# Kernel optimization log

Measured on AMD Instinct MI355X. Metric: run time of the kernel, lower is better.

## Reference

```python
import jax, jax.numpy as jnp
import numpy as np

D = 1024        # n_embed
POS = 512       # n_pos_embed
H = 16          # heads
HS = D // H     # head size
DFF = 4 * D     # mlp hidden
EPS = 1e-5


def layernorm(x, g, b, eps=EPS):
    mu = jnp.mean(x, axis=-1, keepdims=True)
    var = jnp.var(x, axis=-1, keepdims=True)
    return (x - mu) * jax.lax.rsqrt(var + eps) * g + b


def setup_inputs() -> dict:
    key = jax.random.key(0)
    ks = jax.random.split(key, 12)
    std = 0.02
    inp = {
        "grid": jax.random.normal(ks[0], (8, 24, 24, D), dtype=jnp.float32),
        "query_pos": jax.random.normal(ks[1], (8, 1024, POS), dtype=jnp.float32),
        "Wq": jax.random.normal(ks[2], (POS, D), dtype=jnp.float32) * std,
        "Wk": jax.random.normal(ks[3], (D, D), dtype=jnp.float32) * std,
        "Wv": jax.random.normal(ks[4], (D, D), dtype=jnp.float32) * std,
        "Wo": jax.random.normal(ks[5], (D, D), dtype=jnp.float32) * std,
        "ln_grid_g": jnp.ones((D,), jnp.float32),
        "ln_grid_b": jnp.zeros((D,), jnp.float32),
        "ln_q_g": jnp.ones((POS,), jnp.float32),
        "ln_q_b": jnp.zeros((POS,), jnp.float32),
        "ln_mlp_g": jnp.ones((D,), jnp.float32),
        "ln_mlp_b": jnp.zeros((D,), jnp.float32),
        "W1": jax.random.normal(ks[6], (D, DFF), dtype=jnp.float32) * std,
        "b1": jnp.zeros((DFF,), jnp.float32),
        "W2": jax.random.normal(ks[7], (DFF, D), dtype=jnp.float32) * std,
        "b2": jnp.zeros((D,), jnp.float32),
    }
    return inp


def reference(grid, query_pos, Wq, Wk, Wv, Wo, ln_grid_g, ln_grid_b,
              ln_q_g, ln_q_b, ln_mlp_g, ln_mlp_b, W1, b1, W2, b2):
    B, N, M, d = grid.shape
    T = N * M
    grid_flat = grid.reshape(B, T, d)
    grid_norm = layernorm(grid_flat, ln_grid_g, ln_grid_b)
    K = jnp.einsum('btd,de->bte', grid_norm, Wk)
    V = jnp.einsum('btd,de->bte', grid_norm, Wv)
    query_norm = layernorm(query_pos, ln_q_g, ln_q_b)
    Q = jnp.einsum('blp,pe->ble', query_norm, Wq)
    L = Q.shape[1]
    # split heads: (B, H, L, HS)
    Qh = Q.reshape(B, L, H, HS).transpose(0, 2, 1, 3)
    Kh = K.reshape(B, T, H, HS).transpose(0, 2, 1, 3)
    Vh = V.reshape(B, T, H, HS).transpose(0, 2, 1, 3)
    scale = 1.0 / np.sqrt(HS).astype(np.float32)
    scores = jnp.einsum('bhld,bhmd->bhlm', Qh, Kh) * scale
    probs = jax.nn.softmax(scores, axis=-1)
    attn = jnp.einsum('bhlm,bhmd->bhld', probs, Vh)
    attn = attn.transpose(0, 2, 1, 3).reshape(B, L, d)
    attn = jnp.einsum('bld,de->ble', attn, Wo)
    x = Q + attn  # Q_proj residual
    x_norm = layernorm(x, ln_mlp_g, ln_mlp_b)
    mlp = jax.nn.gelu(x_norm @ W1 + b1) @ W2 + b2
    return x + mlp
```

## Files before the change

kernel.cpp:

```cpp
#include <hip/hip_runtime.h>

typedef __bf16 bf16x8 __attribute__((ext_vector_type(8)));
typedef float  f32x4  __attribute__((ext_vector_type(4)));
typedef short  s16x8  __attribute__((ext_vector_type(8)));

__device__ __forceinline__ unsigned short f2b(float f) {
  unsigned int u = __float_as_uint(f);
  u += 0x7fffu + ((u >> 16) & 1u);
  return (unsigned short)(u >> 16);
}
__device__ __forceinline__ float b2f(unsigned short h) {
  return __uint_as_float(((unsigned int)h) << 16);
}

__device__ __forceinline__ void gload_lds16(const unsigned short* g, unsigned short* l) {
  __builtin_amdgcn_global_load_lds((const __attribute__((address_space(1))) void*)g,
                                   (__attribute__((address_space(3))) void*)l, 16, 0, 0);
}

__device__ __forceinline__ void bar() {
  __builtin_amdgcn_sched_barrier(0);
  asm volatile("" ::: "memory");
  __builtin_amdgcn_s_barrier();
  asm volatile("" ::: "memory");
  __builtin_amdgcn_sched_barrier(0);
}

#define WAIT_LGKM0 do { asm volatile("s_waitcnt lgkmcnt(0)" ::: "memory"); \
                        __builtin_amdgcn_sched_barrier(0); } while (0)

__global__ __launch_bounds__(256) void transpose_w(const float* __restrict__ in,
                                                   unsigned short* __restrict__ out,
                                                   int R, int C) {
  __shared__ float t[32][33];
  int c0 = blockIdx.x * 32, r0 = blockIdx.y * 32;
  int tx = threadIdx.x & 31, ty = threadIdx.x >> 5;
  for (int i = ty; i < 32; i += 8)
    t[i][tx] = in[(size_t)(r0 + i) * C + (c0 + tx)];
  __syncthreads();
  for (int i = ty; i < 32; i += 8)
    out[(size_t)(c0 + i) * R + (r0 + tx)] = f2b(t[tx][i]);
}

__global__ __launch_bounds__(256) void transpose_v(const unsigned short* __restrict__ V,
                                                   unsigned short* __restrict__ Vt) {
  __shared__ unsigned short tile[64][72];
  const int t0 = blockIdx.x * 64;
  const int d0 = blockIdx.y * 64;
  const int b  = blockIdx.z;
  const int tid = threadIdx.x;
  const int r = tid >> 3, c8 = tid & 7;
#pragma unroll
  for (int p = 0; p < 2; ++p) {
    int row = p * 32 + r;
    s16x8 v = *(const s16x8*)(V + ((size_t)(b * 576 + t0 + row) * 1024 + d0 + c8 * 8));
    *(s16x8*)&tile[row][c8 * 8] = v;
  }
  __syncthreads();
#pragma unroll
  for (int p = 0; p < 2; ++p) {
    int drow = p * 32 + r;
    unsigned short tmp[8];
#pragma unroll
    for (int j = 0; j < 8; ++j) tmp[j] = tile[c8 * 8 + j][drow];
    *(s16x8*)(Vt + ((size_t)(b * 1024 + d0 + drow) * 576 + t0 + c8 * 8)) = *(const s16x8*)tmp;
  }
}

__global__ __launch_bounds__(256) void ln_kernel(const float* __restrict__ in,
                                                 const float* __restrict__ g,
                                                 const float* __restrict__ b,
                                                 unsigned short* __restrict__ out,
                                                 int cols) {
  int row = blockIdx.x;
  const float* x = in + (size_t)row * cols;
  float s = 0.f, s2 = 0.f;
  for (int c = threadIdx.x * 4; c < cols; c += 1024) {
    float4 v = *(const float4*)(x + c);
    s  += v.x + v.y + v.z + v.w;
    s2 += v.x * v.x + v.y * v.y + v.z * v.z + v.w * v.w;
  }
#pragma unroll
  for (int o = 32; o > 0; o >>= 1) { s += __shfl_down(s, o); s2 += __shfl_down(s2, o); }
  __shared__ float rs[4], rs2[4];
  int w = threadIdx.x >> 6;
  if ((threadIdx.x & 63) == 0) { rs[w] = s; rs2[w] = s2; }
  __syncthreads();
  s  = rs[0] + rs[1] + rs[2] + rs[3];
  s2 = rs2[0] + rs2[1] + rs2[2] + rs2[3];
  float inv  = 1.f / (float)cols;
  float mean = s * inv;
  float var  = s2 * inv - mean * mean;
  float rstd = rsqrtf(var + 1e-5f);
  unsigned short* outp = out + (size_t)row * cols;
  for (int c = threadIdx.x * 4; c < cols; c += 1024) {
    float4 v = *(const float4*)(x + c);
    ushort4 ov;
    ov.x = f2b((v.x - mean) * rstd * g[c + 0] + b[c + 0]);
    ov.y = f2b((v.y - mean) * rstd * g[c + 1] + b[c + 1]);
    ov.z = f2b((v.z - mean) * rstd * g[c + 2] + b[c + 2]);
    ov.w = f2b((v.w - mean) * rstd * g[c + 3] + b[c + 3]);
    *(ushort4*)(outp + c) = ov;
  }
}

template <int BM, int BIAS, int GELU, int RES, int WF32, int WBF16>
__global__ __launch_bounds__(512) void gemm256(const unsigned short* __restrict__ A,
                                               const unsigned short* __restrict__ Bt,
                                               float* __restrict__ Cf,
                                               unsigned short* __restrict__ Cb,
                                               const float* __restrict__ bias,
                                               const float* __restrict__ res,
                                               int M, int N, int K) {
  constexpr int MF = BM / 32;
  constexpr int MH = MF / 2;
  constexpr int LA = BM / 128;
  __shared__ unsigned short L[2][(BM + 256) * 64];
  const int tid = threadIdx.x;
  const int w = tid >> 6, l = tid & 63;
  const int rl = l & 15, kb = l >> 4;
  const int wm = w >> 2, wn = w & 3;
  const int m0 = blockIdx.x * BM, n0 = blockIdx.y * 256;
  const int NT = K >> 6;
  const int colsw = ((l & 7) ^ (l >> 3)) * 8;
  const int lrow = l >> 3;

  auto stage = [&](int t, int half) {
    if (t >= NT) return;
    unsigned short* base = L[t & 1];
    if (half < 2) {
      const unsigned short* g = Bt + (size_t)(n0 + half * 128) * K + t * 64;
#pragma unroll
      for (int j = 0; j < 2; ++j) {
        int row = w * 16 + j * 8;
        gload_lds16(g + (size_t)(row + lrow) * K + colsw,
                    base + BM * 64 + half * 8192 + row * 64);
      }
    } else {
      const int h = half - 2;
      const unsigned short* g = A + (size_t)(m0 + h * (BM / 2)) * K + t * 64;
#pragma unroll
      for (int j = 0; j < LA; ++j) {
        int row = w * (8 * LA) + j * 8;
        gload_lds16(g + (size_t)(row + lrow) * K + colsw,
                    base + h * (BM / 2) * 64 + row * 64);
      }
    }
  };

  f32x4 acc[MF][4];
  f32x4 zz = {0.f, 0.f, 0.f, 0.f};
#pragma unroll
  for (int i = 0; i < MF; ++i)
#pragma unroll
    for (int j = 0; j < 4; ++j) acc[i][j] = zz;

  stage(0, 0); stage(0, 1); stage(0, 2); stage(0, 3);
  stage(1, 0); stage(1, 1); stage(1, 2);

  const int aoff = wm * (BM / 2) * 64;
  const int boff = BM * 64 + (wn >> 1) * 8192 + (wn & 1) * 64 * 64;

  for (int t = 0; t < NT; ++t) {
    const unsigned short* Lb = L[t & 1];
    if (t + 1 < NT) {
      if constexpr (LA == 2) asm volatile("s_waitcnt vmcnt(6)" ::: "memory");
      else                   asm volatile("s_waitcnt vmcnt(5)" ::: "memory");
    } else {
      asm volatile("s_waitcnt vmcnt(0)" ::: "memory");
    }
    __builtin_amdgcn_sched_barrier(0);
    bar();

    bf16x8 af[MH][2], bf[4][2];
#pragma unroll
    for (int mf = 0; mf < MH; ++mf)
#pragma unroll
      for (int kf = 0; kf < 2; ++kf)
        af[mf][kf] = *(const bf16x8*)(Lb + aoff + (mf * 16 + rl) * 64 +
                                      (((kf * 4 + kb) ^ (rl & 7)) * 8));
#pragma unroll
    for (int nf = 0; nf < 4; ++nf)
#pragma unroll
      for (int kf = 0; kf < 2; ++kf)
        bf[nf][kf] = *(const bf16x8*)(Lb + boff + (nf * 16 + rl) * 64 +
                                      (((kf * 4 + kb) ^ (rl & 7)) * 8));
    stage(t + 1, 3);
    WAIT_LGKM0;
    __builtin_amdgcn_s_setprio(1);
#pragma unroll
    for (int mf = 0; mf < MH; ++mf)
#pragma unroll
      for (int nf = 0; nf < 2; ++nf)
#pragma unroll
        for (int kf = 0; kf < 2; ++kf)
          acc[mf][nf] = __builtin_amdgcn_mfma_f32_16x16x32_bf16(af[mf][kf], bf[nf][kf], acc[mf][nf], 0, 0, 0);
    __builtin_amdgcn_s_setprio(0);
    bar();

    stage(t + 2, 0);
    __builtin_amdgcn_s_setprio(1);
#pragma unroll
    for (int mf = 0; mf < MH; ++mf)
#pragma unroll
      for (int nf = 2; nf < 4; ++nf)
#pragma unroll
        for (int kf = 0; kf < 2; ++kf)
          acc[mf][nf] = __builtin_amdgcn_mfma_f32_16x16x32_bf16(af[mf][kf], bf[nf][kf], acc[mf][nf], 0, 0, 0);
    __builtin_amdgcn_s_setprio(0);
    bar();

#pragma unroll
    for (int mf = 0; mf < MH; ++mf)
#pragma unroll
      for (int kf = 0; kf < 2; ++kf)
        af[mf][kf] = *(const bf16x8*)(Lb + aoff + ((MH + mf) * 16 + rl) * 64 +
                                      (((kf * 4 + kb) ^ (rl & 7)) * 8));
    stage(t + 2, 1);
    WAIT_LGKM0;
    __builtin_amdgcn_s_setprio(1);
#pragma unroll
    for (int mf = 0; mf < MH; ++mf)
#pragma unroll
      for (int nf = 0; nf < 2; ++nf)
#pragma unroll
        for (int kf = 0; kf < 2; ++kf)
          acc[MH + mf][nf] = __builtin_amdgcn_mfma_f32_16x16x32_bf16(af[mf][kf], bf[nf][kf], acc[MH + mf][nf], 0, 0, 0);
    __builtin_amdgcn_s_setprio(0);
    bar();

    stage(t + 2, 2);
    __builtin_amdgcn_s_setprio(1);
#pragma unroll
    for (int mf = 0; mf < MH; ++mf)
#pragma unroll
      for (int nf = 2; nf < 4; ++nf)
#pragma unroll
        for (int kf = 0; kf < 2; ++kf)
          acc[MH + mf][nf] = __builtin_amdgcn_mfma_f32_16x16x32_bf16(af[mf][kf], bf[nf][kf], acc[MH + mf][nf], 0, 0, 0);
    __builtin_amdgcn_s_setprio(0);
  }

#pragma unroll
  for (int mf = 0; mf < MF; ++mf) {
#pragma unroll
    for (int nf = 0; nf < 4; ++nf) {
#pragma unroll
      for (int r = 0; r < 4; ++r) {
        int row = m0 + wm * (BM / 2) + mf * 16 + kb * 4 + r;
        int col = n0 + wn * 64 + nf * 16 + rl;
        float v = acc[mf][nf][r];
        if (BIAS) v += bias[col];
        if (GELU) {
          float t2 = 1.5957691f * (v + 0.044715f * v * v * v);
          float e = __expf(fminf(t2, 60.f));
          v = v * e / (e + 1.f);
        }
        if (RES) v += res[(size_t)row * N + col];
        if (WF32) Cf[(size_t)row * N + col] = v;
        if (WBF16) Cb[(size_t)row * N + col] = f2b(v);
      }
    }
  }
}

__global__ __launch_bounds__(256) void attn_mfma(const unsigned short* __restrict__ Qb,
                                                 const unsigned short* __restrict__ Kb,
                                                 const unsigned short* __restrict__ Vtb,
                                                 unsigned short* __restrict__ Ob) {
  __shared__ unsigned short Qs[64 * 64];
  __shared__ unsigned short Ks[2][64 * 64];
  __shared__ unsigned short Vs[2][64 * 64];
  __shared__ unsigned short Ps[64 * 64];

  const int t = threadIdx.x, w = t >> 6, l = t & 63;
  const int b = blockIdx.z, h = blockIdx.y, q0 = blockIdx.x * 64;
  const int rl = l & 15, kb = l >> 4;

  auto stage64 = [&](unsigned short* lds, const unsigned short* g, int gstride) {
#pragma unroll
    for (int p = 0; p < 2; ++p) {
      int row = p * 32 + w * 8 + (l >> 3);
      const unsigned short* src = g + (size_t)row * gstride + (((l & 7) ^ (row & 7)) * 8);
      gload_lds16(src, lds + p * 2048 + w * 512);
    }
  };

  const unsigned short* Qg = Qb + ((size_t)(b * 1024 + q0) * 1024 + h * 64);
  auto Kg = [&](int kt) { return Kb + ((size_t)(b * 576 + kt * 64) * 1024 + h * 64); };
  auto Vg = [&](int kt) { return Vtb + ((size_t)(b * 1024 + h * 64) * 576 + kt * 64); };

  stage64(Qs, Qg, 1024);
  stage64(Ks[0], Kg(0), 1024);
  stage64(Vs[0], Vg(0), 576);
  __syncthreads();

  bf16x8 qf[2];
  {
    int row = w * 16 + rl;
#pragma unroll
    for (int kf = 0; kf < 2; ++kf)
      qf[kf] = *(const bf16x8*)(Qs + row * 64 + (((kf * 4 + kb) ^ (row & 7)) * 8));
  }

  float m_run[4], l_run[4];
  f32x4 accO[4];
#pragma unroll
  for (int r = 0; r < 4; ++r) { m_run[r] = -1e30f; l_run[r] = 0.f; }
  f32x4 zz = {0.f, 0.f, 0.f, 0.f};
#pragma unroll
  for (int nf = 0; nf < 4; ++nf) accO[nf] = zz;

  for (int kt = 0; kt < 9; ++kt) {
    const int buf = kt & 1;
    if (kt + 1 < 9) {
      stage64(Ks[buf ^ 1], Kg(kt + 1), 1024);
      stage64(Vs[buf ^ 1], Vg(kt + 1), 576);
    }

    f32x4 accS[4];
#pragma unroll
    for (int nf = 0; nf < 4; ++nf) accS[nf] = zz;
#pragma unroll
    for (int nf = 0; nf < 4; ++nf) {
      int row = nf * 16 + rl;
#pragma unroll
      for (int kf = 0; kf < 2; ++kf) {
        bf16x8 kfrag = *(const bf16x8*)(Ks[buf] + row * 64 + (((kf * 4 + kb) ^ (row & 7)) * 8));
        accS[nf] = __builtin_amdgcn_mfma_f32_16x16x32_bf16(qf[kf], kfrag, accS[nf], 0, 0, 0);
      }
    }

    float sv[4][4];
#pragma unroll
    for (int nf = 0; nf < 4; ++nf)
#pragma unroll
      for (int r = 0; r < 4; ++r) sv[nf][r] = accS[nf][r] * 0.125f;

    float al[4];
#pragma unroll
    for (int r = 0; r < 4; ++r) {
      float mr = fmaxf(fmaxf(sv[0][r], sv[1][r]), fmaxf(sv[2][r], sv[3][r]));
#pragma unroll
      for (int xm = 1; xm < 16; xm <<= 1) mr = fmaxf(mr, __shfl_xor(mr, xm));
      float mn = fmaxf(m_run[r], mr);
      al[r] = __expf(m_run[r] - mn);
      m_run[r] = mn;
      float rs = 0.f;
#pragma unroll
      for (int nf = 0; nf < 4; ++nf) {
        sv[nf][r] = __expf(sv[nf][r] - mn);
        rs += sv[nf][r];
      }
#pragma unroll
      for (int xm = 1; xm < 16; xm <<= 1) rs += __shfl_xor(rs, xm);
      l_run[r] = l_run[r] * al[r] + rs;
    }

#pragma unroll
    for (int nf = 0; nf < 4; ++nf)
#pragma unroll
      for (int r = 0; r < 4; ++r) {
        int q = w * 16 + kb * 4 + r;
        int col = nf * 16 + rl;
        Ps[q * 64 + (col ^ ((q & 7) << 3))] = f2b(sv[nf][r]);
      }

#pragma unroll
    for (int nf = 0; nf < 4; ++nf)
#pragma unroll
      for (int r = 0; r < 4; ++r) accO[nf][r] *= al[r];

    asm volatile("s_waitcnt lgkmcnt(0)" ::: "memory");
    __builtin_amdgcn_sched_barrier(0);

    bf16x8 pf[2];
    {
      int row = w * 16 + rl;
#pragma unroll
      for (int kf = 0; kf < 2; ++kf)
        pf[kf] = *(const bf16x8*)(Ps + row * 64 + (((kf * 4 + kb) ^ (row & 7)) * 8));
    }
#pragma unroll
    for (int nf = 0; nf < 4; ++nf) {
      int row = nf * 16 + rl;
#pragma unroll
      for (int kf = 0; kf < 2; ++kf) {
        bf16x8 vfrag = *(const bf16x8*)(Vs[buf] + row * 64 + (((kf * 4 + kb) ^ (row & 7)) * 8));
        accO[nf] = __builtin_amdgcn_mfma_f32_16x16x32_bf16(pf[kf], vfrag, accO[nf], 0, 0, 0);
      }
    }

    __syncthreads();
  }

#pragma unroll
  for (int nf = 0; nf < 4; ++nf) {
#pragma unroll
    for (int r = 0; r < 4; ++r) {
      float o = accO[nf][r] / l_run[r];
      size_t qg = (size_t)(b * 1024 + q0 + w * 16 + kb * 4 + r);
      Ob[qg * 1024 + h * 64 + nf * 16 + rl] = f2b(o);
    }
  }
}

extern "C" void kernel_launch(void* const* d_in, const int* in_sizes, int n_in,
                              void* d_out, int out_size, void* d_ws, size_t ws_size,
                              hipStream_t stream) {
  const float* grid_in = (const float*)d_in[0];
  const float* qpos    = (const float*)d_in[1];
  const float* Wq      = (const float*)d_in[2];
  const float* Wk      = (const float*)d_in[3];
  const float* Wv      = (const float*)d_in[4];
  const float* Wo      = (const float*)d_in[5];
  const float* g_grid  = (const float*)d_in[6];
  const float* b_grid  = (const float*)d_in[7];
  const float* g_q     = (const float*)d_in[8];
  const float* b_q     = (const float*)d_in[9];
  const float* g_mlp   = (const float*)d_in[10];
  const float* b_mlp   = (const float*)d_in[11];
  const float* W1      = (const float*)d_in[12];
  const float* b1      = (const float*)d_in[13];
  const float* W2      = (const float*)d_in[14];
  const float* b2      = (const float*)d_in[15];

  char* ws = (char*)d_ws;
  size_t off = 0;
  auto alloc = [&](size_t bytes) -> void* {
    void* p = ws + off;
    off = (off + bytes + 255) & ~(size_t)255;
    return p;
  };

  unsigned short* Wqt = (unsigned short*)alloc((size_t)1024 * 512 * 2);
  unsigned short* Wkt = (unsigned short*)alloc((size_t)1024 * 1024 * 2);
  unsigned short* Wvt = (unsigned short*)alloc((size_t)1024 * 1024 * 2);
  unsigned short* Wot = (unsigned short*)alloc((size_t)1024 * 1024 * 2);
  unsigned short* W1t = (unsigned short*)alloc((size_t)4096 * 1024 * 2);
  unsigned short* W2t = (unsigned short*)alloc((size_t)1024 * 4096 * 2);
  unsigned short* gn  = (unsigned short*)alloc((size_t)4608 * 1024 * 2);
  unsigned short* qn  = (unsigned short*)alloc((size_t)8192 * 512 * 2);
  unsigned short* Kb  = (unsigned short*)alloc((size_t)4608 * 1024 * 2);
  unsigned short* Vb  = (unsigned short*)alloc((size_t)4608 * 1024 * 2);
  float*          Qf  = (float*)alloc((size_t)8192 * 1024 * 4);
  unsigned short* Qbf = (unsigned short*)alloc((size_t)8192 * 1024 * 2);
  unsigned short* atb = (unsigned short*)alloc((size_t)8192 * 1024 * 2);
  float*          xf  = (float*)alloc((size_t)8192 * 1024 * 4);
  unsigned short* xnb = (unsigned short*)alloc((size_t)8192 * 1024 * 2);
  unsigned short* hb  = (unsigned short*)alloc((size_t)8192 * 4096 * 2);
  unsigned short* Vtb = hb;
  (void)ws_size; (void)in_sizes; (void)n_in; (void)out_size;

  transpose_w<<<dim3(32, 16), 256, 0, stream>>>(Wq, Wqt, 512, 1024);
  transpose_w<<<dim3(32, 32), 256, 0, stream>>>(Wk, Wkt, 1024, 1024);
  transpose_w<<<dim3(32, 32), 256, 0, stream>>>(Wv, Wvt, 1024, 1024);
  transpose_w<<<dim3(32, 32), 256, 0, stream>>>(Wo, Wot, 1024, 1024);
  transpose_w<<<dim3(128, 32), 256, 0, stream>>>(W1, W1t, 1024, 4096);
  transpose_w<<<dim3(32, 128), 256, 0, stream>>>(W2, W2t, 4096, 1024);

  ln_kernel<<<4608, 256, 0, stream>>>(grid_in, g_grid, b_grid, gn, 1024);
  ln_kernel<<<8192, 256, 0, stream>>>(qpos, g_q, b_q, qn, 512);

  gemm256<128, 0, 0, 0, 0, 1><<<dim3(36, 4), 512, 0, stream>>>(gn, Wkt, nullptr, Kb, nullptr, nullptr, 4608, 1024, 1024);
  gemm256<128, 0, 0, 0, 0, 1><<<dim3(36, 4), 512, 0, stream>>>(gn, Wvt, nullptr, Vb, nullptr, nullptr, 4608, 1024, 1024);
  gemm256<128, 0, 0, 0, 1, 1><<<dim3(64, 4), 512, 0, stream>>>(qn, Wqt, Qf, Qbf, nullptr, nullptr, 8192, 1024, 512);

  transpose_v<<<dim3(9, 16, 8), 256, 0, stream>>>(Vb, Vtb);

  attn_mfma<<<dim3(16, 16, 8), 256, 0, stream>>>(Qbf, Kb, Vtb, atb);

  gemm256<128, 0, 0, 1, 1, 0><<<dim3(64, 4), 512, 0, stream>>>(atb, Wot, xf, nullptr, nullptr, Qf, 8192, 1024, 1024);

  ln_kernel<<<8192, 256, 0, stream>>>(xf, g_mlp, b_mlp, xnb, 1024);
  gemm256<256, 1, 1, 0, 0, 1><<<dim3(32, 16), 512, 0, stream>>>(xnb, W1t, nullptr, hb, b1, nullptr, 8192, 4096, 1024);
  gemm256<128, 1, 0, 1, 1, 0><<<dim3(64, 4), 512, 0, stream>>>(hb, W2t, (float*)d_out, nullptr, b2, xf, 8192, 1024, 4096);
}
```

Baseline: 378.3 us.

## Stage GEMM epilogue through LDS for vector stores, fuse K/V GEMM, drop fp32 Q

The GEMM epilogue now writes each 16x64 per-wave patch into LDS and re-reads it so that global stores, and residual loads, use 16-byte vectors instead of scattered scalar accesses. Bias is hoisted into registers. The K and V projections are merged into one GEMM over a concatenated weight, with strided access in transpose_v and attention. The fp32 Q output is dropped and the Wo residual is read from bf16 Q, which cuts memory traffic but lowers the precision of the residual path.

```diff
diff --git a/kernel.cpp b/kernel.cpp
--- a/kernel.cpp
+++ b/kernel.cpp
@@ -43,7 +43,8 @@
 }
 
 __global__ __launch_bounds__(256) void transpose_v(const unsigned short* __restrict__ V,
-                                                   unsigned short* __restrict__ Vt) {
+                                                   unsigned short* __restrict__ Vt,
+                                                   int vstride) {
   __shared__ unsigned short tile[64][72];
   const int t0 = blockIdx.x * 64;
   const int d0 = blockIdx.y * 64;
@@ -53,7 +54,7 @@
 #pragma unroll
   for (int p = 0; p < 2; ++p) {
     int row = p * 32 + r;
-    s16x8 v = *(const s16x8*)(V + ((size_t)(b * 576 + t0 + row) * 1024 + d0 + c8 * 8));
+    s16x8 v = *(const s16x8*)(V + ((size_t)(b * 576 + t0 + row) * vstride + d0 + c8 * 8));
     *(s16x8*)&tile[row][c8 * 8] = v;
   }
   __syncthreads();
@@ -104,13 +105,14 @@
   }
 }
 
-template <int BM, int BIAS, int GELU, int RES, int WF32, int WBF16>
+template <int BM, int BIAS, int GELU, int RES, int OUTBF>
 __global__ __launch_bounds__(512) void gemm256(const unsigned short* __restrict__ A,
                                                const unsigned short* __restrict__ Bt,
                                                float* __restrict__ Cf,
                                                unsigned short* __restrict__ Cb,
                                                const float* __restrict__ bias,
-                                               const float* __restrict__ res,
+                                               const float* __restrict__ resf,
+                                               const unsigned short* __restrict__ resb,
                                                int M, int N, int K) {
   constexpr int MF = BM / 32;
   constexpr int MH = MF / 2;
@@ -241,33 +243,73 @@
     __builtin_amdgcn_s_setprio(0);
   }
 
+  bar();
+
+  float bias_v[4];
+  if (BIAS) {
+#pragma unroll
+    for (int nf = 0; nf < 4; ++nf) bias_v[nf] = bias[n0 + wn * 64 + nf * 16 + rl];
+  }
+  unsigned short* patch  = ((unsigned short*)L) + w * (16 * 72);
+  float*          patchf = ((float*)L) + w * (16 * 72);
+
 #pragma unroll
   for (int mf = 0; mf < MF; ++mf) {
 #pragma unroll
     for (int nf = 0; nf < 4; ++nf) {
 #pragma unroll
       for (int r = 0; r < 4; ++r) {
-        int row = m0 + wm * (BM / 2) + mf * 16 + kb * 4 + r;
-        int col = n0 + wn * 64 + nf * 16 + rl;
         float v = acc[mf][nf][r];
-        if (BIAS) v += bias[col];
+        if (BIAS) v += bias_v[nf];
         if (GELU) {
           float t2 = 1.5957691f * (v + 0.044715f * v * v * v);
           float e = __expf(fminf(t2, 60.f));
           v = v * e / (e + 1.f);
         }
-        if (RES) v += res[(size_t)row * N + col];
-        if (WF32) Cf[(size_t)row * N + col] = v;
-        if (WBF16) Cb[(size_t)row * N + col] = f2b(v);
-      }
-    }
+        int prow = kb * 4 + r, pcol = nf * 16 + rl;
+        if (OUTBF) patch[prow * 72 + pcol] = f2b(v);
+        else       patchf[prow * 72 + pcol] = v;
+      }
+    }
+    WAIT_LGKM0;
+    if (OUTBF) {
+#pragma unroll
+      for (int half = 0; half < 2; ++half) {
+        int prow = half * 8 + (l >> 3);
+        int pcol = (l & 7) * 8;
+        s16x8 vv = *(const s16x8*)(patch + prow * 72 + pcol);
+        int grow = m0 + wm * (BM / 2) + mf * 16 + prow;
+        int gcol = n0 + wn * 64 + pcol;
+        *(s16x8*)(Cb + (size_t)grow * N + gcol) = vv;
+      }
+    } else {
+#pragma unroll
+      for (int p = 0; p < 4; ++p) {
+        int prow = p * 4 + (l >> 4);
+        int pcol = (l & 15) * 4;
+        float4 vv = *(const float4*)(patchf + prow * 72 + pcol);
+        int grow = m0 + wm * (BM / 2) + mf * 16 + prow;
+        int gcol = n0 + wn * 64 + pcol;
+        if (RES == 1) {
+          float4 rv = *(const float4*)(resf + (size_t)grow * N + gcol);
+          vv.x += rv.x; vv.y += rv.y; vv.z += rv.z; vv.w += rv.w;
+        }
+        if (RES == 2) {
+          ushort4 rv = *(const ushort4*)(resb + (size_t)grow * N + gcol);
+          vv.x += b2f(rv.x); vv.y += b2f(rv.y); vv.z += b2f(rv.z); vv.w += b2f(rv.w);
+        }
+        *(float4*)(Cf + (size_t)grow * N + gcol) = vv;
+      }
+    }
+    WAIT_LGKM0;
   }
 }
 
 __global__ __launch_bounds__(256) void attn_mfma(const unsigned short* __restrict__ Qb,
                                                  const unsigned short* __restrict__ Kb,
                                                  const unsigned short* __restrict__ Vtb,
-                                                 unsigned short* __restrict__ Ob) {
+                                                 unsigned short* __restrict__ Ob,
+                                                 int kstride) {
   __shared__ unsigned short Qs[64 * 64];
   __shared__ unsigned short Ks[2][64 * 64];
   __shared__ unsigned short Vs[2][64 * 64];
@@ -287,11 +329,11 @@
   };
 
   const unsigned short* Qg = Qb + ((size_t)(b * 1024 + q0) * 1024 + h * 64);
-  auto Kg = [&](int kt) { return Kb + ((size_t)(b * 576 + kt * 64) * 1024 + h * 64); };
+  auto Kg = [&](int kt) { return Kb + ((size_t)(b * 576 + kt * 64) * kstride + h * 64); };
   auto Vg = [&](int kt) { return Vtb + ((size_t)(b * 1024 + h * 64) * 576 + kt * 64); };
 
   stage64(Qs, Qg, 1024);
-  stage64(Ks[0], Kg(0), 1024);
+  stage64(Ks[0], Kg(0), kstride);
   stage64(Vs[0], Vg(0), 576);
   __syncthreads();
 
@@ -314,7 +356,7 @@
   for (int kt = 0; kt < 9; ++kt) {
     const int buf = kt & 1;
     if (kt + 1 < 9) {
-      stage64(Ks[buf ^ 1], Kg(kt + 1), 1024);
+      stage64(Ks[buf ^ 1], Kg(kt + 1), kstride);
       stage64(Vs[buf ^ 1], Vg(kt + 1), 576);
     }
 
@@ -433,28 +475,25 @@
     return p;
   };
 
-  unsigned short* Wqt = (unsigned short*)alloc((size_t)1024 * 512 * 2);
-  unsigned short* Wkt = (unsigned short*)alloc((size_t)1024 * 1024 * 2);
-  unsigned short* Wvt = (unsigned short*)alloc((size_t)1024 * 1024 * 2);
-  unsigned short* Wot = (unsigned short*)alloc((size_t)1024 * 1024 * 2);
-  unsigned short* W1t = (unsigned short*)alloc((size_t)4096 * 1024 * 2);
-  unsigned short* W2t = (unsigned short*)alloc((size_t)1024 * 4096 * 2);
-  unsigned short* gn  = (unsigned short*)alloc((size_t)4608 * 1024 * 2);
-  unsigned short* qn  = (unsigned short*)alloc((size_t)8192 * 512 * 2);
-  unsigned short* Kb  = (unsigned short*)alloc((size_t)4608 * 1024 * 2);
-  unsigned short* Vb  = (unsigned short*)alloc((size_t)4608 * 1024 * 2);
-  float*          Qf  = (float*)alloc((size_t)8192 * 1024 * 4);
-  unsigned short* Qbf = (unsigned short*)alloc((size_t)8192 * 1024 * 2);
-  unsigned short* atb = (unsigned short*)alloc((size_t)8192 * 1024 * 2);
-  float*          xf  = (float*)alloc((size_t)8192 * 1024 * 4);
-  unsigned short* xnb = (unsigned short*)alloc((size_t)8192 * 1024 * 2);
-  unsigned short* hb  = (unsigned short*)alloc((size_t)8192 * 4096 * 2);
-  unsigned short* Vtb = hb;
+  unsigned short* Wqt  = (unsigned short*)alloc((size_t)1024 * 512 * 2);
+  unsigned short* Wkvt = (unsigned short*)alloc((size_t)2048 * 1024 * 2);
+  unsigned short* Wot  = (unsigned short*)alloc((size_t)1024 * 1024 * 2);
+  unsigned short* W1t  = (unsigned short*)alloc((size_t)4096 * 1024 * 2);
+  unsigned short* W2t  = (unsigned short*)alloc((size_t)1024 * 4096 * 2);
+  unsigned short* gn   = (unsigned short*)alloc((size_t)4608 * 1024 * 2);
+  unsigned short* qn   = (unsigned short*)alloc((size_t)8192 * 512 * 2);
+  unsigned short* KVb  = (unsigned short*)alloc((size_t)4608 * 2048 * 2);
+  unsigned short* Qbf  = (unsigned short*)alloc((size_t)8192 * 1024 * 2);
+  unsigned short* atb  = (unsigned short*)alloc((size_t)8192 * 1024 * 2);
+  float*          xf   = (float*)alloc((size_t)8192 * 1024 * 4);
+  unsigned short* xnb  = (unsigned short*)alloc((size_t)8192 * 1024 * 2);
+  unsigned short* hb   = (unsigned short*)alloc((size_t)8192 * 4096 * 2);
+  unsigned short* Vtb  = hb;
   (void)ws_size; (void)in_sizes; (void)n_in; (void)out_size;
 
   transpose_w<<<dim3(32, 16), 256, 0, stream>>>(Wq, Wqt, 512, 1024);
-  transpose_w<<<dim3(32, 32), 256, 0, stream>>>(Wk, Wkt, 1024, 1024);
-  transpose_w<<<dim3(32, 32), 256, 0, stream>>>(Wv, Wvt, 1024, 1024);
+  transpose_w<<<dim3(32, 32), 256, 0, stream>>>(Wk, Wkvt, 1024, 1024);
+  transpose_w<<<dim3(32, 32), 256, 0, stream>>>(Wv, Wkvt + (size_t)1024 * 1024, 1024, 1024);
   transpose_w<<<dim3(32, 32), 256, 0, stream>>>(Wo, Wot, 1024, 1024);
   transpose_w<<<dim3(128, 32), 256, 0, stream>>>(W1, W1t, 1024, 4096);
   transpose_w<<<dim3(32, 128), 256, 0, stream>>>(W2, W2t, 4096, 1024);
@@ -462,17 +501,16 @@
   ln_kernel<<<4608, 256, 0, stream>>>(grid_in, g_grid, b_grid, gn, 1024);
   ln_kernel<<<8192, 256, 0, stream>>>(qpos, g_q, b_q, qn, 512);
 
-  gemm256<128, 0, 0, 0, 0, 1><<<dim3(36, 4), 512, 0, stream>>>(gn, Wkt, nullptr, Kb, nullptr, nullptr, 4608, 1024, 1024);
-  gemm256<128, 0, 0, 0, 0, 1><<<dim3(36, 4), 512, 0, stream>>>(gn, Wvt, nullptr, Vb, nullptr, nullptr, 4608, 1024, 1024);
-  gemm256<128, 0, 0, 0, 1, 1><<<dim3(64, 4), 512, 0, stream>>>(qn, Wqt, Qf, Qbf, nullptr, nullptr, 8192, 1024, 512);
-
-  transpose_v<<<dim3(9, 16, 8), 256, 0, stream>>>(Vb, Vtb);
-
-  attn_mfma<<<dim3(16, 16, 8), 256, 0, stream>>>(Qbf, Kb, Vtb, atb);
-
-  gemm256<128, 0, 0, 1, 1, 0><<<dim3(64, 4), 512, 0, stream>>>(atb, Wot, xf, nullptr, nullptr, Qf, 8192, 1024, 1024);
+  gemm256<128, 0, 0, 0, 1><<<dim3(36, 8), 512, 0, stream>>>(gn, Wkvt, nullptr, KVb, nullptr, nullptr, nullptr, 4608, 2048, 1024);
+  gemm256<128, 0, 0, 0, 1><<<dim3(64, 4), 512, 0, stream>>>(qn, Wqt, nullptr, Qbf, nullptr, nullptr, nullptr, 8192, 1024, 512);
+
+  transpose_v<<<dim3(9, 16, 8), 256, 0, stream>>>(KVb + 1024, Vtb, 2048);
+
+  attn_mfma<<<dim3(16, 16, 8), 256, 0, stream>>>(Qbf, KVb, Vtb, atb, 2048);
+
+  gemm256<128, 0, 0, 2, 0><<<dim3(64, 4), 512, 0, stream>>>(atb, Wot, xf, nullptr, nullptr, nullptr, Qbf, 8192, 1024, 1024);
 
   ln_kernel<<<8192, 256, 0, stream>>>(xf, g_mlp, b_mlp, xnb, 1024);
-  gemm256<256, 1, 1, 0, 0, 1><<<dim3(32, 16), 512, 0, stream>>>(xnb, W1t, nullptr, hb, b1, nullptr, 8192, 4096, 1024);
-  gemm256<128, 1, 0, 1, 1, 0><<<dim3(64, 4), 512, 0, stream>>>(hb, W2t, (float*)d_out, nullptr, b2, xf, 8192, 1024, 4096);
-}
+  gemm256<256, 1, 1, 0, 1><<<dim3(32, 16), 512, 0, stream>>>(xnb, W1t, nullptr, hb, b1, nullptr, nullptr, 8192, 4096, 1024);
+  gemm256<128, 1, 0, 1, 0><<<dim3(64, 4), 512, 0, stream>>>(hb, W2t, (float*)d_out, nullptr, b2, xf, nullptr, 8192, 1024, 4096);
+}
```

After: 368.6 us. -2.6%, faster.
